# Kernel optimization log

Hardware: AMD Instinct MI355X
Metric: run time of the kernel (lower is better)

The kernel has to match this reference:

```python
import jax, jax.numpy as jnp
import numpy as np

C = 256  # channels
SHAPES = [(8, C, 80, 80), (8, C, 40, 40), (8, C, 20, 20), (8, C, 10, 10)]
EPS = 1e-8  # torch cosine_similarity eps


def _nearest_resize(x, H, W):
    # Matches F.interpolate(mode='nearest'): src_idx = floor(dst_idx * in/out)
    b, c, h, w = x.shape
    rows = (jnp.arange(H) * h) // H
    cols = (jnp.arange(W) * w) // W
    return x[:, :, rows[:, None], cols[None, :]]


def setup_inputs() -> dict:
    key = jax.random.key(0)
    ks = jax.random.split(key, 12)
    d = {}
    for i, s in enumerate(SHAPES):
        d[f"f{i}"] = jax.random.normal(ks[i], s, dtype=jnp.float32)
        d[f"w{i}"] = jax.random.normal(ks[4 + i], (C, C), dtype=jnp.float32) / jnp.sqrt(jnp.float32(C))
        d[f"b{i}"] = jax.random.normal(ks[8 + i], (C,), dtype=jnp.float32) * 0.01
    return d


def reference(f0, f1, f2, f3, w0, w1, w2, w3, b0, b1, b2, b3):
    feats = [f0, f1, f2, f3]
    ws = [w0, w1, w2, w3]
    bs = [b0, b1, b2, b3]
    H = max(f.shape[2] for f in feats)
    W = max(f.shape[3] for f in feats)
    proj = []
    for f, w, b in zip(feats, ws, bs):
        # 1x1 conv == per-pixel GEMM over channels
        p = jnp.einsum('bchw,oc->bohw', f, w) + b[None, :, None, None]
        if p.shape[2] != H or p.shape[3] != W:
            p = _nearest_resize(p, H, W)
        proj.append(p)
    B = proj[0].shape[0]
    N = len(proj)
    x = jnp.stack(proj, axis=1).reshape(B, N, C, H * W)  # [B,N,C,L]
    # Pairwise cosine similarity along channel dim at each spatial location,
    # then mean over locations (vectorized form of the O(N^2) torch loop).
    dot = jnp.einsum('bicl,bjcl->bijl', x, x)            # [B,N,N,L]
    nrm = jnp.sqrt(jnp.einsum('bicl,bicl->bil', x, x))   # [B,N,L]
    denom = jnp.maximum(nrm[:, :, None, :] * nrm[:, None, :, :], EPS)
    attn = (dot / denom).mean(axis=-1)                   # [B,N,N]
    return jax.nn.softmax(attn, axis=-1)
```

## Files before the change

### kernel.cpp

```cpp
#include <hip/hip_runtime.h>


#define CCH 256

typedef __attribute__((ext_vector_type(8))) short short8;
typedef __attribute__((ext_vector_type(4))) float float4_;

__device__ inline short f2bf(float x) {
    union { float f; unsigned u; } c; c.f = x;
    unsigned u = c.u + 0x7FFFu + ((c.u >> 16) & 1u);
    return (short)(u >> 16);
}
__device__ inline float bf2f(short b) {
    union { unsigned u; float f; } c; c.u = ((unsigned)(unsigned short)b) << 16;
    return c.f;
}

__global__ void pack_w(const float* __restrict__ w0, const float* __restrict__ w1,
                       const float* __restrict__ w2, const float* __restrict__ w3,
                       short* __restrict__ wp) {
    const float* W[4] = {w0, w1, w2, w3};
    const float* Ws = W[blockIdx.y];
    short* out = wp + (size_t)blockIdx.y * 65536;
    int base = (blockIdx.x * 256 + threadIdx.x) * 8;
    int kk0 = base & 31;
    int o   = (base >> 5) & 255;
    int ks  = base >> 13;
    const float* src = Ws + o * CCH + ks * 32 + kk0;
    short8 v;
#pragma unroll
    for (int j = 0; j < 8; ++j) v[j] = f2bf(src[j]);
    *(short8*)(out + base) = v;
}

#define LDP 56
__global__ __launch_bounds__(256) void proj_norm(
    const float* __restrict__ f0, const float* __restrict__ f1,
    const float* __restrict__ f2, const float* __restrict__ f3,
    const short* __restrict__ wp,
    const float* __restrict__ b0, const float* __restrict__ b1,
    const float* __restrict__ b2, const float* __restrict__ b3,
    short* __restrict__ u0, short* __restrict__ u1,
    short* __restrict__ u2, short* __restrict__ u3)
{
    __shared__ short Wt[256 * LDP];
    __shared__ short Ft[64 * LDP];
    __shared__ float biasS[256];

    const int blk = blockIdx.x;
    int s, b, tile, L;
    const float* F; const float* bias; short* U;
    if (blk < 800)       { s = 0; int r = blk;        b = r / 100; tile = r % 100; L = 6400; F = f0; bias = b0; U = u0; }
    else if (blk < 1000) { s = 1; int r = blk - 800;  b = r / 25;  tile = r % 25;  L = 1600; F = f1; bias = b1; U = u1; }
    else if (blk < 1056) { s = 2; int r = blk - 1000; b = r / 7;   tile = r % 7;   L = 400;  F = f2; bias = b2; U = u2; }
    else                 { s = 3; int r = blk - 1056; b = r / 2;   tile = r % 2;   L = 100;  F = f3; bias = b3; U = u3; }

    const int t    = threadIdx.x;
    const int lane = t & 63;
    const int wav  = t >> 6;
    const int ln   = lane & 15;
    const int quad = lane >> 4;
    const int pixbase = tile * 64;
    const float* Fb = F + (size_t)b * CCH * L;
    const short* wbase = wp + (size_t)s * 65536;

    biasS[t] = bias[t];

    float4_ acc[16];
#pragma unroll
    for (int i = 0; i < 16; ++i) acc[i] = (float4_){0.f, 0.f, 0.f, 0.f};

    const int fpix = t & 63;
    const int fk0  = (t >> 6) * 8;
    const int gpix = pixbase + fpix;
    const bool pin = gpix < L;

    for (int ks = 0; ks < 8; ++ks) {
        __syncthreads();
        {
            const short8* src = (const short8*)(wbase + ks * 8192);
#pragma unroll
            for (int it = 0; it < 4; ++it) {
                int idx = it * 256 + t;
                short8 v = src[idx];
                *(short8*)(&Wt[(idx >> 2) * LDP + (idx & 3) * 8]) = v;
            }
        }
        {
            const float* fs = Fb + (size_t)(ks * 32 + fk0) * L + gpix;
            short8 v;
#pragma unroll
            for (int j = 0; j < 8; ++j)
                v[j] = f2bf(pin ? fs[(size_t)j * L] : 0.f);
            *(short8*)(&Ft[fpix * LDP + fk0]) = v;
        }
        __syncthreads();
        short8 bfrag = *(const short8*)(&Ft[(wav * 16 + ln) * LDP + quad * 8]);
#pragma unroll
        for (int mt = 0; mt < 16; ++mt) {
            short8 afrag = *(const short8*)(&Wt[(mt * 16 + ln) * LDP + quad * 8]);
            acc[mt] = __builtin_amdgcn_mfma_f32_16x16x32_bf16(afrag, bfrag, acc[mt], 0, 0, 0);
        }
    }

    const int mygp = pixbase + wav * 16 + ln;
    float ss = 0.f;
#pragma unroll
    for (int mt = 0; mt < 16; ++mt) {
#pragma unroll
        for (int r = 0; r < 4; ++r) {
            float v = acc[mt][r] + biasS[mt * 16 + quad * 4 + r];
            acc[mt][r] = v;
            ss += v * v;
        }
    }
    ss += __shfl_xor(ss, 16);
    ss += __shfl_xor(ss, 32);
    const float inv = 1.f / sqrtf(fmaxf(ss, 1e-24f));
    if (mygp < L) {
        short* Ub = U + (size_t)b * CCH * L + mygp;
#pragma unroll
        for (int mt = 0; mt < 16; ++mt) {
#pragma unroll
            for (int r = 0; r < 4; ++r)
                Ub[(size_t)(mt * 16 + quad * 4 + r) * L] = f2bf(acc[mt][r] * inv);
        }
    }
}

__global__ void pair_cos(const short* __restrict__ u0, const short* __restrict__ u1,
                         const short* __restrict__ u2, const short* __restrict__ u3,
                         float* __restrict__ partial) {
    const int pair = blockIdx.y;
    const int b = blockIdx.z;
    int i, j;
    switch (pair) {
        case 0: i = 0; j = 1; break;
        case 1: i = 0; j = 2; break;
        case 2: i = 0; j = 3; break;
        case 3: i = 1; j = 2; break;
        case 4: i = 1; j = 3; break;
        default: i = 2; j = 3; break;
    }
    const short* P[4] = {u0, u1, u2, u3};
    const short* pi = P[i];
    const short* pj = P[j];
    const int ri = 80 >> i, rj = 80 >> j;
    const int Li = ri * ri, Lj = rj * rj;

    int pix = blockIdx.x * 256 + threadIdx.x;
    float dot = 0.f;
    if (pix < Li) {
        int h = pix / ri, w = pix - h * ri;
        int d = j - i;
        int l2 = (h >> d) * rj + (w >> d);
        const short* a  = pi + (size_t)b * CCH * Li + pix;
        const short* bb = pj + (size_t)b * CCH * Lj + l2;
#pragma unroll 4
        for (int c = 0; c < CCH; ++c)
            dot += bf2f(a[(size_t)c * Li]) * bf2f(bb[(size_t)c * Lj]);
    }

    __shared__ float red[256];
    red[threadIdx.x] = dot;
    __syncthreads();
    for (int s2 = 128; s2 > 0; s2 >>= 1) {
        if (threadIdx.x < s2) red[threadIdx.x] += red[threadIdx.x + s2];
        __syncthreads();
    }
    if (threadIdx.x == 0) partial[(b * 6 + pair) * 25 + blockIdx.x] = red[0];
}

__global__ void softmax4(const float* __restrict__ partial, float* __restrict__ out) {
    int t = threadIdx.x;
    if (t >= 128) return;
    int b = t >> 4, i = (t >> 2) & 3, j = t & 3;
    float a[4];
#pragma unroll
    for (int jj = 0; jj < 4; ++jj) {
        if (jj == i) { a[jj] = 1.0f; continue; }
        int lo = i < jj ? i : jj;
        int hi = i < jj ? jj : i;
        int pidx;
        if (lo == 0) pidx = hi - 1;
        else if (lo == 1) pidx = 1 + hi;
        else pidx = 5;
        float s = 0.f;
        for (int k = 0; k < 25; ++k) s += partial[(b * 6 + pidx) * 25 + k];
        int rf = 80 >> lo;
        a[jj] = s / (float)(rf * rf);
    }
    float m = fmaxf(fmaxf(a[0], a[1]), fmaxf(a[2], a[3]));
    float e0 = expf(a[0] - m), e1 = expf(a[1] - m), e2 = expf(a[2] - m), e3 = expf(a[3] - m);
    float sum = e0 + e1 + e2 + e3;
    float ev = (j == 0) ? e0 : (j == 1) ? e1 : (j == 2) ? e2 : e3;
    out[t] = ev / sum;
}

extern "C" void kernel_launch(void* const* d_in, const int* in_sizes, int n_in,
                              void* d_out, int out_size, void* d_ws, size_t ws_size,
                              hipStream_t stream) {
    const float* f[4]  = {(const float*)d_in[0], (const float*)d_in[3],
                          (const float*)d_in[6], (const float*)d_in[9]};
    const float* w[4]  = {(const float*)d_in[1], (const float*)d_in[4],
                          (const float*)d_in[7], (const float*)d_in[10]};
    const float* bs[4] = {(const float*)d_in[2], (const float*)d_in[5],
                          (const float*)d_in[8], (const float*)d_in[11]};

    const int Ls[4] = {6400, 1600, 400, 100};
    char* ws = (char*)d_ws;
    size_t off = 0;
    short* u[4];
    for (int s = 0; s < 4; ++s) {
        u[s] = (short*)(ws + off);
        off += (size_t)8 * CCH * Ls[s] * sizeof(short);
    }
    short* wp = (short*)(ws + off); off += 4 * 65536 * sizeof(short);
    float* partial = (float*)(ws + off);

    pack_w<<<dim3(32, 4), 256, 0, stream>>>(w[0], w[1], w[2], w[3], wp);

    proj_norm<<<1072, 256, 0, stream>>>(f[0], f[1], f[2], f[3], wp,
                                        bs[0], bs[1], bs[2], bs[3],
                                        u[0], u[1], u[2], u[3]);

    pair_cos<<<dim3(25, 6, 8), 256, 0, stream>>>(u[0], u[1], u[2], u[3], partial);

    softmax4<<<1, 128, 0, stream>>>(partial, (float*)d_out);
}
```

Baseline: 177.8 us.

## Store normalized projections pixel-major and fuse pair dots per source scale

```diff
diff --git a/kernel.cpp b/kernel.cpp
--- a/kernel.cpp
+++ b/kernel.cpp
@@ -4,6 +4,7 @@
 #define CCH 256
 
 typedef __attribute__((ext_vector_type(8))) short short8;
+typedef __attribute__((ext_vector_type(4))) short short4_;
 typedef __attribute__((ext_vector_type(4))) float float4_;
 
 __device__ inline short f2bf(float x) {
@@ -33,8 +34,8 @@
     *(short8*)(out + base) = v;
 }
 
-#define LDP 56
-__global__ __launch_bounds__(256) void proj_norm(
+#define TPITCH 264
+__global__ __launch_bounds__(256) void proj_norm2(
     const float* __restrict__ f0, const float* __restrict__ f1,
     const float* __restrict__ f2, const float* __restrict__ f3,
     const short* __restrict__ wp,
@@ -43,9 +44,7 @@
     short* __restrict__ u0, short* __restrict__ u1,
     short* __restrict__ u2, short* __restrict__ u3)
 {
-    __shared__ short Wt[256 * LDP];
-    __shared__ short Ft[64 * LDP];
-    __shared__ float biasS[256];
+    __shared__ short Ut[64 * TPITCH];
 
     const int blk = blockIdx.x;
     int s, b, tile, L;
@@ -64,52 +63,36 @@
     const float* Fb = F + (size_t)b * CCH * L;
     const short* wbase = wp + (size_t)s * 65536;
 
-    biasS[t] = bias[t];
+    const int gpix = pixbase + wav * 16 + ln;
+    const bool pin = gpix < L;
+    const int gl = pin ? gpix : 0;
 
     float4_ acc[16];
 #pragma unroll
     for (int i = 0; i < 16; ++i) acc[i] = (float4_){0.f, 0.f, 0.f, 0.f};
 
-    const int fpix = t & 63;
-    const int fk0  = (t >> 6) * 8;
-    const int gpix = pixbase + fpix;
-    const bool pin = gpix < L;
-
     for (int ks = 0; ks < 8; ++ks) {
-        __syncthreads();
-        {
-            const short8* src = (const short8*)(wbase + ks * 8192);
-#pragma unroll
-            for (int it = 0; it < 4; ++it) {
-                int idx = it * 256 + t;
-                short8 v = src[idx];
-                *(short8*)(&Wt[(idx >> 2) * LDP + (idx & 3) * 8]) = v;
-            }
-        }
-        {
-            const float* fs = Fb + (size_t)(ks * 32 + fk0) * L + gpix;
-            short8 v;
-#pragma unroll
-            for (int j = 0; j < 8; ++j)
-                v[j] = f2bf(pin ? fs[(size_t)j * L] : 0.f);
-            *(short8*)(&Ft[fpix * LDP + fk0]) = v;
-        }
-        __syncthreads();
-        short8 bfrag = *(const short8*)(&Ft[(wav * 16 + ln) * LDP + quad * 8]);
+        const float* fs = Fb + (size_t)(ks * 32 + quad * 8) * L + gl;
+        short8 bfrag;
+#pragma unroll
+        for (int j = 0; j < 8; ++j) {
+            float x = fs[(size_t)j * L];
+            bfrag[j] = pin ? f2bf(x) : (short)0;
+        }
 #pragma unroll
         for (int mt = 0; mt < 16; ++mt) {
-            short8 afrag = *(const short8*)(&Wt[(mt * 16 + ln) * LDP + quad * 8]);
+            short8 afrag = *(const short8*)(wbase + ks * 8192 + (mt * 16 + ln) * 32 + quad * 8);
             acc[mt] = __builtin_amdgcn_mfma_f32_16x16x32_bf16(afrag, bfrag, acc[mt], 0, 0, 0);
         }
     }
 
-    const int mygp = pixbase + wav * 16 + ln;
     float ss = 0.f;
 #pragma unroll
     for (int mt = 0; mt < 16; ++mt) {
+        float4_ bv = *(const float4_*)(bias + mt * 16 + quad * 4);
 #pragma unroll
         for (int r = 0; r < 4; ++r) {
-            float v = acc[mt][r] + biasS[mt * 16 + quad * 4 + r];
+            float v = acc[mt][r] + bv[r];
             acc[mt][r] = v;
             ss += v * v;
         }
@@ -117,61 +100,107 @@
     ss += __shfl_xor(ss, 16);
     ss += __shfl_xor(ss, 32);
     const float inv = 1.f / sqrtf(fmaxf(ss, 1e-24f));
-    if (mygp < L) {
-        short* Ub = U + (size_t)b * CCH * L + mygp;
-#pragma unroll
-        for (int mt = 0; mt < 16; ++mt) {
-#pragma unroll
-            for (int r = 0; r < 4; ++r)
-                Ub[(size_t)(mt * 16 + quad * 4 + r) * L] = f2bf(acc[mt][r] * inv);
-        }
-    }
-}
-
-__global__ void pair_cos(const short* __restrict__ u0, const short* __restrict__ u1,
-                         const short* __restrict__ u2, const short* __restrict__ u3,
-                         float* __restrict__ partial) {
-    const int pair = blockIdx.y;
+
+    const int pxl = wav * 16 + ln;
+#pragma unroll
+    for (int mt = 0; mt < 16; ++mt) {
+        short4_ v;
+#pragma unroll
+        for (int r = 0; r < 4; ++r) v[r] = f2bf(acc[mt][r] * inv);
+        *(short4_*)(&Ut[pxl * TPITCH + mt * 16 + quad * 4]) = v;
+    }
+    __syncthreads();
+
+    {
+        const int opx = t >> 2;
+        const int c0 = (t & 3) * 64;
+        const int gpx = pixbase + opx;
+        if (gpx < L) {
+            short* dst = U + ((size_t)b * L + gpx) * CCH + c0;
+#pragma unroll
+            for (int k = 0; k < 8; ++k)
+                *(short8*)(dst + k * 8) = *(const short8*)(&Ut[opx * TPITCH + c0 + k * 8]);
+        }
+    }
+}
+
+template <int I>
+__device__ inline void pair_body(const short* __restrict__ ui,
+                                 const short* __restrict__ uu1,
+                                 const short* __restrict__ uu2,
+                                 const short* __restrict__ uu3,
+                                 int b, int wave_id, int pg, int sub, float* acc) {
+    constexpr int RI = 80 >> I;
+    constexpr int LI = RI * RI;
+    constexpr int NG = LI / 8;
+    const short* __restrict__ uj[3] = {uu1, uu2, uu3};
+
+    for (int g = wave_id; g < NG; g += 200) {
+        const int px = g * 8 + pg;
+        const int h = px / RI;
+        const int w = px - h * RI;
+        const short* pa = ui + ((size_t)(b * LI + px)) * CCH + sub * 32;
+        float a[32];
+#pragma unroll
+        for (int k = 0; k < 4; ++k) {
+            short8 v = *(const short8*)(pa + k * 8);
+#pragma unroll
+            for (int e = 0; e < 8; ++e) a[k * 8 + e] = bf2f(v[e]);
+        }
+#pragma unroll
+        for (int d = 1; d <= 3 - I; ++d) {
+            const int RJ = RI >> d;
+            const int LJ = RJ * RJ;
+            const int pxj = (h >> d) * RJ + (w >> d);
+            const short* pb = uj[d - 1] + ((size_t)(b * LJ + pxj)) * CCH + sub * 32;
+            float s = 0.f;
+#pragma unroll
+            for (int k = 0; k < 4; ++k) {
+                short8 v = *(const short8*)(pb + k * 8);
+#pragma unroll
+                for (int e = 0; e < 8; ++e) s += a[k * 8 + e] * bf2f(v[e]);
+            }
+            acc[d - 1] += s;
+        }
+    }
+}
+
+__global__ __launch_bounds__(256) void pair_dots(
+    const short* __restrict__ u0, const short* __restrict__ u1,
+    const short* __restrict__ u2, const short* __restrict__ u3,
+    float* __restrict__ sums) {
+    const int i = blockIdx.y;
     const int b = blockIdx.z;
-    int i, j;
-    switch (pair) {
-        case 0: i = 0; j = 1; break;
-        case 1: i = 0; j = 2; break;
-        case 2: i = 0; j = 3; break;
-        case 3: i = 1; j = 2; break;
-        case 4: i = 1; j = 3; break;
-        default: i = 2; j = 3; break;
-    }
-    const short* P[4] = {u0, u1, u2, u3};
-    const short* pi = P[i];
-    const short* pj = P[j];
-    const int ri = 80 >> i, rj = 80 >> j;
-    const int Li = ri * ri, Lj = rj * rj;
-
-    int pix = blockIdx.x * 256 + threadIdx.x;
-    float dot = 0.f;
-    if (pix < Li) {
-        int h = pix / ri, w = pix - h * ri;
-        int d = j - i;
-        int l2 = (h >> d) * rj + (w >> d);
-        const short* a  = pi + (size_t)b * CCH * Li + pix;
-        const short* bb = pj + (size_t)b * CCH * Lj + l2;
-#pragma unroll 4
-        for (int c = 0; c < CCH; ++c)
-            dot += bf2f(a[(size_t)c * Li]) * bf2f(bb[(size_t)c * Lj]);
-    }
-
-    __shared__ float red[256];
-    red[threadIdx.x] = dot;
+    const int t = threadIdx.x;
+    const int lane = t & 63;
+    const int wav = t >> 6;
+    const int wave_id = blockIdx.x * 4 + wav;
+    const int pg = lane >> 3;
+    const int sub = lane & 7;
+
+    float acc[3] = {0.f, 0.f, 0.f};
+    if (i == 0)      pair_body<0>(u0, u1, u2, u3, b, wave_id, pg, sub, acc);
+    else if (i == 1) pair_body<1>(u1, u2, u3, u3, b, wave_id, pg, sub, acc);
+    else             pair_body<2>(u2, u3, u3, u3, b, wave_id, pg, sub, acc);
+
+    __shared__ float red[4][3];
+#pragma unroll
+    for (int p = 0; p < 3; ++p) {
+        float v = acc[p];
+        v += __shfl_xor(v, 1);  v += __shfl_xor(v, 2);  v += __shfl_xor(v, 4);
+        v += __shfl_xor(v, 8);  v += __shfl_xor(v, 16); v += __shfl_xor(v, 32);
+        if (lane == 0) red[wav][p] = v;
+    }
     __syncthreads();
-    for (int s2 = 128; s2 > 0; s2 >>= 1) {
-        if (threadIdx.x < s2) red[threadIdx.x] += red[threadIdx.x + s2];
-        __syncthreads();
-    }
-    if (threadIdx.x == 0) partial[(b * 6 + pair) * 25 + blockIdx.x] = red[0];
-}
-
-__global__ void softmax4(const float* __restrict__ partial, float* __restrict__ out) {
+    const int npairs = 3 - i;
+    const int base = (i == 0) ? 0 : (i == 1) ? 3 : 5;
+    if (t < npairs) {
+        float s = red[0][t] + red[1][t] + red[2][t] + red[3][t];
+        atomicAdd(&sums[b * 6 + base + t], s);
+    }
+}
+
+__global__ void softmax4(const float* __restrict__ sums, float* __restrict__ out) {
     int t = threadIdx.x;
     if (t >= 128) return;
     int b = t >> 4, i = (t >> 2) & 3, j = t & 3;
@@ -185,10 +214,8 @@
         if (lo == 0) pidx = hi - 1;
         else if (lo == 1) pidx = 1 + hi;
         else pidx = 5;
-        float s = 0.f;
-        for (int k = 0; k < 25; ++k) s += partial[(b * 6 + pidx) * 25 + k];
         int rf = 80 >> lo;
-        a[jj] = s / (float)(rf * rf);
+        a[jj] = sums[b * 6 + pidx] / (float)(rf * rf);
     }
     float m = fmaxf(fmaxf(a[0], a[1]), fmaxf(a[2], a[3]));
     float e0 = expf(a[0] - m), e1 = expf(a[1] - m), e2 = expf(a[2] - m), e3 = expf(a[3] - m);
@@ -216,15 +243,17 @@
         off += (size_t)8 * CCH * Ls[s] * sizeof(short);
     }
     short* wp = (short*)(ws + off); off += 4 * 65536 * sizeof(short);
-    float* partial = (float*)(ws + off);
+    float* sums = (float*)(ws + off);
+
+    hipMemsetAsync(sums, 0, 64 * sizeof(float), stream);
 
     pack_w<<<dim3(32, 4), 256, 0, stream>>>(w[0], w[1], w[2], w[3], wp);
 
-    proj_norm<<<1072, 256, 0, stream>>>(f[0], f[1], f[2], f[3], wp,
-                                        bs[0], bs[1], bs[2], bs[3],
-                                        u[0], u[1], u[2], u[3]);
-
-    pair_cos<<<dim3(25, 6, 8), 256, 0, stream>>>(u[0], u[1], u[2], u[3], partial);
-
-    softmax4<<<1, 128, 0, stream>>>(partial, (float*)d_out);
-}
+    proj_norm2<<<1072, 256, 0, stream>>>(f[0], f[1], f[2], f[3], wp,
+                                         bs[0], bs[1], bs[2], bs[3],
+                                         u[0], u[1], u[2], u[3]);
+
+    pair_dots<<<dim3(50, 3, 8), 256, 0, stream>>>(u[0], u[1], u[2], u[3], sums);
+
+    softmax4<<<1, 128, 0, stream>>>(sums, (float*)d_out);
+}
```

Result: slower. 253.5 us (+42.6%).
